# Kernel optimization log

Measured on AMD Instinct MI355X. Metric: run time of the kernel, lower is better.

Reference implementation:

```python
import jax, jax.numpy as jnp
import numpy as np

NUM_CAPS = 16; PLANES = 16; CAPS_SIZE = 16; NUM_CLASSES = 10
MAT = 4; ITERS = 3; FINAL_LAMBDA = 1e-2; EPS = 1e-8; BN_EPS = 1e-5
LN_2PI = float(np.log(2.0 * np.pi))


def _conv(x, w, pad):
    return jax.lax.conv_general_dilated(x, w, (1, 1), ((pad, pad), (pad, pad)),
                                        dimension_numbers=('NCHW', 'OIHW', 'NCHW'))


def _bn(x, g, b, m, v):
    # inference-mode BatchNorm2d
    scale = g / jnp.sqrt(v + BN_EPS)
    return (x - m[None, :, None, None]) * scale[None, :, None, None] + b[None, :, None, None]


def _unfold(x, k, stride, pad):
    # torch F.unfold ordering: [b, c, k*k, l]
    b, c, h, w = x.shape
    xp = jnp.pad(x, ((0, 0), (0, 0), (pad, pad), (pad, pad)))
    oh = (h + 2 * pad - k) // stride + 1
    ow = (w + 2 * pad - k) // stride + 1
    cols = jnp.stack([xp[:, :, i:i + stride * (oh - 1) + 1:stride, j:j + stride * (ow - 1) + 1:stride]
                      for i in range(k) for j in range(k)], axis=2)  # [b,c,kk,oh,ow]
    return cols.reshape(b, c, k * k, oh * ow), oh, ow


def em_routing(a, pose, W, beta_u, beta_a, k, stride, pad, A, B, P):
    mat = int(P ** 0.5); b = a.shape[0]; kk = k * k
    pc, oh, ow = _unfold(pose, k, stride, pad)          # [b, A*P, kk, l]
    l = oh * ow
    pc = pc.reshape(b, A, P, kk, l)
    pc = jnp.transpose(pc, (0, 4, 3, 1, 2)).reshape(b, l, kk * A, mat, mat)
    # votes: [b, l, kkA, B, P]
    v = jnp.einsum('blkih,kohj->blkoij', pc, W).reshape(b, l, kk * A, B, P)
    ac, _, _ = _unfold(a, k, stride, pad)               # [b, A, kk, l]
    a_in = jnp.transpose(ac.reshape(b, A, kk, l), (0, 3, 2, 1)).reshape(b, l, kk * A, 1)
    bu = beta_u.reshape(1, 1, 1, B, 1)
    ba = beta_a.reshape(1, 1, 1, B)
    r = jnp.full((b, l, kk * A, B), 1.0 / B, dtype=a.dtype)
    for it in range(ITERS):
        lam = FINAL_LAMBDA * (1.0 - 0.95 ** (it + 1))
        # ---- M step ----
        rw = r * a_in
        rw = rw / (jnp.sum(rw, axis=3, keepdims=True) + EPS)
        r_sum = jnp.sum(rw, axis=2, keepdims=True)            # [b,l,1,B]
        coeff = (rw / (r_sum + EPS))[..., None]
        mu = jnp.sum(coeff * v, axis=2, keepdims=True)        # [b,l,1,B,P]
        sig = jnp.sum(coeff * (v - mu) ** 2, axis=2, keepdims=True) + EPS
        cost = (bu + 0.5 * jnp.log(sig)) * r_sum[..., None]
        a_out = jax.nn.sigmoid(lam * (ba - jnp.sum(cost, axis=4)))  # [b,l,1,B]
        # ---- E step ----
        if it < ITERS - 1:
            ln_p = -0.5 * (v - mu) ** 2 / sig - 0.5 * jnp.log(sig) - 0.5 * LN_2PI
            r = jax.nn.softmax(jnp.sum(ln_p, axis=4) + jnp.log(a_out), axis=3)
    a_map = jnp.transpose(a_out.reshape(b, oh, ow, B), (0, 3, 1, 2))
    pose_map = jnp.transpose(mu.reshape(b, oh, ow, B * P), (0, 3, 1, 2))
    return a_map, pose_map


def setup_inputs() -> dict:
    key = jax.random.key(0)
    ks = jax.random.split(key, 24)
    Bt = 32; C_in = NUM_CAPS * PLANES  # 256
    d = {}
    d['x'] = jax.random.normal(ks[0], (Bt, C_in, 8, 8), jnp.float32)
    d['conv_a_w'] = jax.random.normal(ks[1], (NUM_CAPS, C_in, 3, 3), jnp.float32) * 0.03
    d['conv_pose_w'] = jax.random.normal(ks[2], (NUM_CAPS * CAPS_SIZE, C_in, 3, 3), jnp.float32) * 0.03

    def bn_params(k1, k2, c):
        return (jnp.ones((c,), jnp.float32), jnp.zeros((c,), jnp.float32),
                jax.random.normal(k1, (c,), jnp.float32) * 0.1,
                1.0 + 0.1 * jax.random.uniform(k2, (c,), jnp.float32))
    d['bn_a_g'], d['bn_a_b'], d['bn_a_m'], d['bn_a_v'] = bn_params(ks[3], ks[4], NUM_CAPS)
    d['bn_pose_g'], d['bn_pose_b'], d['bn_pose_m'], d['bn_pose_v'] = bn_params(ks[5], ks[6], NUM_CAPS * CAPS_SIZE)
    kkA = 9 * NUM_CAPS
    d['em0_W'] = jax.random.uniform(ks[7], (kkA, NUM_CAPS, MAT, MAT), jnp.float32, -0.5, 0.5)
    d['em0_bu'] = jax.random.normal(ks[8], (NUM_CAPS,), jnp.float32) * 0.01
    d['em0_ba'] = jax.random.normal(ks[9], (NUM_CAPS,), jnp.float32) * 0.01
    d['bn0_g'], d['bn0_b'], d['bn0_m'], d['bn0_v'] = bn_params(ks[10], ks[11], NUM_CAPS * CAPS_SIZE)
    d['em1_W'] = jax.random.uniform(ks[12], (kkA, NUM_CAPS, MAT, MAT), jnp.float32, -0.5, 0.5)
    d['em1_bu'] = jax.random.normal(ks[13], (NUM_CAPS,), jnp.float32) * 0.01
    d['em1_ba'] = jax.random.normal(ks[14], (NUM_CAPS,), jnp.float32) * 0.01
    d['bn1_g'], d['bn1_b'], d['bn1_m'], d['bn1_v'] = bn_params(ks[15], ks[16], NUM_CAPS * CAPS_SIZE)
    d['fc_W'] = jax.random.uniform(ks[17], (16 * NUM_CAPS, NUM_CLASSES, MAT, MAT), jnp.float32, -0.5, 0.5)
    d['fc_bu'] = jax.random.normal(ks[18], (NUM_CLASSES,), jnp.float32) * 0.01
    d['fc_ba'] = jax.random.normal(ks[19], (NUM_CLASSES,), jnp.float32) * 0.01
    return d


def reference(x, conv_a_w, conv_pose_w, bn_a_g, bn_a_b, bn_a_m, bn_a_v,
              bn_pose_g, bn_pose_b, bn_pose_m, bn_pose_v,
              em0_W, em0_bu, em0_ba, bn0_g, bn0_b, bn0_m, bn0_v,
              em1_W, em1_bu, em1_ba, bn1_g, bn1_b, bn1_m, bn1_v,
              fc_W, fc_bu, fc_ba):
    a = jax.nn.sigmoid(_bn(_conv(x, conv_a_w, 1), bn_a_g, bn_a_b, bn_a_m, bn_a_v))
    pose = _bn(_conv(x, conv_pose_w, 1), bn_pose_g, bn_pose_b, bn_pose_m, bn_pose_v)
    a, pose = em_routing(a, pose, em0_W, em0_bu, em0_ba, 3, 1, 1, NUM_CAPS, NUM_CAPS, CAPS_SIZE)
    pose = _bn(pose, bn0_g, bn0_b, bn0_m, bn0_v)
    a, pose = em_routing(a, pose, em1_W, em1_bu, em1_ba, 3, 1, 1, NUM_CAPS, NUM_CAPS, CAPS_SIZE)
    pose = _bn(pose, bn1_g, bn1_b, bn1_m, bn1_v)
    a, _ = em_routing(a, pose, fc_W, fc_bu, fc_ba, 4, 1, 0, NUM_CAPS, NUM_CLASSES, CAPS_SIZE)
    return jnp.mean(a, axis=(2, 3))  # [B, num_classes]
```

## Files before the change

kernel.cpp:

```cpp
#include <hip/hip_runtime.h>

#define EPSV 1e-8f
#define BN_EPS 1e-5f
#define LN_2PI 1.8378770664093453f

typedef float v2f __attribute__((ext_vector_type(2)));
__device__ __forceinline__ v2f splat2(float x) { v2f r; r.x = x; r.y = x; return r; }

__device__ __forceinline__ float sigmoidf_(float x) { return 1.0f / (1.0f + expf(-x)); }

template<int C>
__device__ __forceinline__ float dppx(float x) {
    int i = __builtin_amdgcn_mov_dpp(__builtin_bit_cast(int, x), C, 0xF, 0xF, true);
    return __builtin_bit_cast(float, i);
}


template<int NACC>
__device__ __forceinline__ void conv3_body(
    const float* __restrict__ x, const float* __restrict__ w,
    const float* __restrict__ g, const float* __restrict__ b_,
    const float* __restrict__ m, const float* __restrict__ v,
    float* __restrict__ out, int OC, int icChunk,
    int bidx, int ocg, int icq, float* xs, int t)
{
    const int pix = t & 63, py = pix >> 3, px = pix & 7;
    const int ocb_u = __builtin_amdgcn_readfirstlane(t >> 6);
    const int ic0 = icq * icChunk;
    const int OCB = 4 * NACC;

    const int cells = icChunk * 120;
    for (int idx = t; idx < cells; idx += 256) {
        int icl = idx / 120;
        int c = idx - icl * 120;
        int iy = c / 12, ix = c - iy * 12;
        float val = 0.f;
        if (iy >= 1 && iy <= 8 && ix >= 1 && ix <= 8)
            val = x[(bidx * 256 + ic0 + icl) * 64 + (iy - 1) * 8 + (ix - 1)];
        xs[idx] = val;
    }
    __syncthreads();

    const int oc_base = ocg * OCB + ocb_u;
    const float* wb = w + ((size_t)(oc_base * 256 + ic0)) * 9;

    float acc[NACC];
    #pragma unroll
    for (int q = 0; q < NACC; ++q) acc[q] = 0.f;

    for (int icl = 0; icl < icChunk; ++icl) {
        const float* xr = &xs[icl * 120 + py * 12 + px];
        const float* wr = &wb[icl * 9];
        #pragma unroll
        for (int ky = 0; ky < 3; ++ky)
            #pragma unroll
            for (int kx = 0; kx < 3; ++kx) {
                float xv = xr[ky * 12 + kx];
                #pragma unroll
                for (int q = 0; q < NACC; ++q)
                    acc[q] = fmaf(wr[q * 9216 + ky * 3 + kx], xv, acc[q]);
            }
    }
    __syncthreads();
    #pragma unroll
    for (int q = 0; q < NACC; ++q) {
        int oc = oc_base + 4 * q;
        float sc = g[oc] * rsqrtf(v[oc] + BN_EPS);
        float add = acc[q] * sc;
        if (icq == 0) add += b_[oc] - m[oc] * sc;
        xs[pix * (OCB + 1) + ocb_u + 4 * q] = add;
    }
    __syncthreads();
    const int per = (64 * OCB) / 256;
    #pragma unroll
    for (int e = 0; e < per; ++e) {
        int idx = t * per + e;
        int pp = idx / OCB, ocl = idx - pp * OCB;
        atomicAdd(&out[(bidx * 64 + pp) * OC + ocg * OCB + ocl], xs[pp * (OCB + 1) + ocl]);
    }
}

__global__ __launch_bounds__(256, 4) void k_conv_fused(
    const float* __restrict__ x,
    const float* __restrict__ wa, const float* __restrict__ ga, const float* __restrict__ bba,
    const float* __restrict__ ma, const float* __restrict__ va, float* __restrict__ outa,
    const float* __restrict__ wp, const float* __restrict__ gp, const float* __restrict__ bbp,
    const float* __restrict__ mp, const float* __restrict__ vp, float* __restrict__ outp)
{
    __shared__ float xs[32 * 120];
    const int t = threadIdx.x;
    const int bid = blockIdx.x;
    if (bid < 256) {
        int bidx = bid >> 3, icq = bid & 7;
        conv3_body<4>(x, wa, ga, bba, ma, va, outa, 16, 32, bidx, 0, icq, xs, t);
    } else {
        int r = bid - 256;
        int bidx = r >> 6, rem = r & 63;
        int ocg = rem >> 3, icq = rem & 7;
        conv3_body<8>(x, wp, gp, bbp, mp, vp, outp, 256, 32, bidx, ocg, icq, xs, t);
    }
}

__global__ __launch_bounds__(768) void k_em_conv(
    const float* __restrict__ a_in, const float* __restrict__ pose_in,
    const float* __restrict__ W, const float* __restrict__ bu, const float* __restrict__ ba,
    const float* __restrict__ bng, const float* __restrict__ bnb,
    const float* __restrict__ bnm, const float* __restrict__ bnv,
    float* __restrict__ a_out_g, float* __restrict__ pose_out, int sig_flag)
{
    __shared__ float4 red4[192 * 9] __attribute__((aligned(16)));
    __shared__ float prsum[192];
    __shared__ float a_s[160];
    __shared__ float mu_s[16 * 18], is_s[16 * 18];
    __shared__ float cst0_s[16], aout_s[16], laout_s[16];

    const int t = threadIdx.x;
    const int bidx = blockIdx.x >> 6;
    const int l = blockIdx.x & 63;
    const int y = l >> 3, xo = l & 7;
    const int kgl = t & 3;
    const int o = (t >> 2) & 15;
    const int w_id = t >> 6;
    const int kg = w_id * 4 + kgl;

    float* pc_s = reinterpret_cast<float*>(red4);

    for (int idx = t; idx < 2304; idx += 768) {
        int kk = idx >> 8, c = idx & 255;
        int k = idx >> 4, p = idx & 15;
        int iy = y + kk / 3 - 1, ix = xo + (kk % 3) - 1;
        float val = 0.f;
        if (iy >= 0 && iy < 8 && ix >= 0 && ix < 8)
            val = pose_in[((bidx * 64 + iy * 8 + ix) << 8) + c];
        pc_s[k * 20 + p] = val;
    }
    if (t < 144) {
        int kk = t >> 4;
        int iy = y + kk / 3 - 1, ix = xo + (kk % 3) - 1;
        float raw = (iy >= 0 && iy < 8 && ix >= 0 && ix < 8)
                    ? a_in[((bidx * 64 + iy * 8 + ix) << 4) + (t & 15)] : 0.f;
        a_s[t] = sig_flag ? sigmoidf_(raw) : raw;
    }
    __syncthreads();

    v2f v2[3][8];
    const float4* W4 = reinterpret_cast<const float4*>(W);
    #pragma unroll
    for (int s = 0; s < 3; ++s) {
        int k = kg + 48 * s;
        float pcl[16];
        #pragma unroll
        for (int c = 0; c < 4; ++c) {
            float4 p4 = *reinterpret_cast<const float4*>(&pc_s[k * 20 + c * 4]);
            pcl[c * 4 + 0] = p4.x; pcl[c * 4 + 1] = p4.y; pcl[c * 4 + 2] = p4.z; pcl[c * 4 + 3] = p4.w;
        }
        #pragma unroll
        for (int j = 0; j < 8; ++j) v2[s][j] = splat2(0.f);
        #pragma unroll
        for (int h = 0; h < 4; ++h) {
            float4 wr = W4[(k * 16 + o) * 4 + h];
            v2f wa; wa.x = wr.x; wa.y = wr.y;
            v2f wb; wb.x = wr.z; wb.y = wr.w;
            #pragma unroll
            for (int i = 0; i < 4; ++i) {
                v2f a2 = splat2(pcl[i * 4 + h]);
                v2[s][i * 2]     += a2 * wa;
                v2[s][i * 2 + 1] += a2 * wb;
            }
        }
    }
    float afac[3];
    #pragma unroll
    for (int s = 0; s < 3; ++s) { float av = a_s[kg + 48 * s]; afac[s] = av / (av + EPSV); }
    __syncthreads();

    float lg[3] = {0.f, 0.f, 0.f};
    for (int it = 0; it < 3; ++it) {
        float lam = (it == 0) ? 5.0e-4f : ((it == 1) ? 9.75e-4f : 1.42625e-3f);
        float rw[3];
        if (it == 0) {
            #pragma unroll
            for (int s = 0; s < 3; ++s) rw[s] = 0.0625f * afac[s];
        } else {
            #pragma unroll
            for (int s = 0; s < 3; ++s) {
                float mx = lg[s];
                #pragma unroll
                for (int mk = 4; mk <= 32; mk <<= 1) mx = fmaxf(mx, __shfl_xor(mx, mk, 64));
                float e = expf(lg[s] - mx);
                float den = e;
                #pragma unroll
                for (int mk = 4; mk <= 32; mk <<= 1) den += __shfl_xor(den, mk, 64);
                rw[s] = (e / den) * afac[s];
            }
        }
        float prw = rw[0] + rw[1] + rw[2];
        prw += dppx<0xB1>(prw); prw += dppx<0x4E>(prw);
        if (kgl == 0) prsum[w_id * 16 + o] = prw;
        const int row4 = (w_id * 16 + o) * 9;
        const v2f r0 = splat2(rw[0]), r1 = splat2(rw[1]), r2 = splat2(rw[2]);
        #pragma unroll
        for (int j = 0; j < 8; ++j) {
            v2f a0 = v2[0][j], a1 = v2[1][j], a2 = v2[2][j];
            v2f pm = r0 * a0 + r1 * a1 + r2 * a2;
            v2f pq = r0 * (a0 * a0) + r1 * (a1 * a1) + r2 * (a2 * a2);
            float pmx = pm.x, pmy = pm.y, pqx = pq.x, pqy = pq.y;
            pmx += dppx<0xB1>(pmx); pmx += dppx<0x4E>(pmx);
            pmy += dppx<0xB1>(pmy); pmy += dppx<0x4E>(pmy);
            pqx += dppx<0xB1>(pqx); pqx += dppx<0x4E>(pqx);
            pqy += dppx<0xB1>(pqy); pqy += dppx<0x4E>(pqy);
            if (kgl == 0) red4[row4 + j] = make_float4(pmx, pmy, pqx, pqy);
        }
        __syncthreads();
        if (t < 256) {
            int oo = t >> 4, p = t & 15;
            int jj = p >> 1, sel = p & 1;
            const float* rf = reinterpret_cast<const float*>(red4);
            float spm = 0.f, spq = 0.f, srs = 0.f;
            #pragma unroll
            for (int u = 0; u < 12; ++u) {
                int base = ((u * 16 + oo) * 9 + jj) * 4;
                spm += rf[base + sel];
                spq += rf[base + 2 + sel];
                srs += prsum[u * 16 + oo];
            }
            float invr = 1.f / (srs + EPSV);
            float mu = spm * invr;
            float beta = srs * invr;
            float sig = fmaf(-(2.f - beta) * mu, mu, spq * invr) + EPSV;
            float ls = logf(sig);
            mu_s[oo * 18 + p] = mu;
            is_s[oo * 18 + p] = 1.f / sig;
            float sumls = ls;
            #pragma unroll
            for (int mk = 1; mk <= 8; mk <<= 1) sumls += __shfl_xor(sumls, mk, 64);
            if (p == 0) {
                float cost = srs * fmaf(0.5f, sumls, 16.f * bu[oo]);
                float ao = sigmoidf_(lam * (ba[oo] - cost));
                aout_s[oo] = ao; laout_s[oo] = logf(ao);
                cst0_s[oo] = fmaf(-0.5f, sumls, -8.f * LN_2PI);
            }
        }
        __syncthreads();
        if (it < 2) {
            const v2f* mu2 = reinterpret_cast<const v2f*>(&mu_s[o * 18]);
            const v2f* is2 = reinterpret_cast<const v2f*>(&is_s[o * 18]);
            v2f s0 = splat2(0.f), s1 = splat2(0.f), s2 = splat2(0.f);
            #pragma unroll
            for (int j = 0; j < 8; ++j) {
                v2f m2 = mu2[j], iv = is2[j];
                v2f d0 = v2[0][j] - m2; s0 += (d0 * d0) * iv;
                v2f d1 = v2[1][j] - m2; s1 += (d1 * d1) * iv;
                v2f d2 = v2[2][j] - m2; s2 += (d2 * d2) * iv;
            }
            float cb = cst0_s[o] + laout_s[o];
            lg[0] = fmaf(-0.5f, s0.x + s0.y, cb);
            lg[1] = fmaf(-0.5f, s1.x + s1.y, cb);
            lg[2] = fmaf(-0.5f, s2.x + s2.y, cb);
        }
    }
    if (t < 256) {
        float sc = bng[t] * rsqrtf(bnv[t] + BN_EPS);
        float mu = mu_s[(t >> 4) * 18 + (t & 15)];
        pose_out[((bidx * 64 + l) << 8) + t] = (mu - bnm[t]) * sc + bnb[t];
    }
    if (t < 16) a_out_g[((bidx * 64 + l) << 4) + t] = aout_s[t];
}

__global__ __launch_bounds__(640) void k_em_fc(
    const float* __restrict__ a_in, const float* __restrict__ pose_in,
    const float* __restrict__ W, const float* __restrict__ bu, const float* __restrict__ ba,
    float* __restrict__ out)
{
    __shared__ float pcs[5120];
    __shared__ float rws[2816];
    __shared__ float ain_s[256];
    __shared__ float mu_s[10 * 18], is_s[10 * 18];

    const int t = threadIdx.x;
    const int bidx = blockIdx.x / 25;
    const int l = blockIdx.x % 25;
    const int y = l / 5, xo = l % 5;
    const int o = t >> 6;
    const int g = t & 63;

    for (int idx = t; idx < 4096; idx += 640) {
        int kk = idx >> 8, c = idx & 255;
        int k = idx >> 4, p = idx & 15;
        int iy = y + (kk >> 2), ix = xo + (kk & 3);
        pcs[k * 20 + p] = pose_in[((bidx * 64 + iy * 8 + ix) << 8) + c];
    }
    if (t < 256) {
        int kk = t >> 4;
        int iy = y + (kk >> 2), ix = xo + (kk & 3);
        ain_s[t] = a_in[((bidx * 64 + iy * 8 + ix) << 4) + (t & 15)];
    }
    __syncthreads();

    v2f v2[4][8];
    const float4* W4 = reinterpret_cast<const float4*>(W);
    #pragma unroll
    for (int s = 0; s < 4; ++s) {
        int k = g + 64 * s;
        float pcl[16];
        #pragma unroll
        for (int c = 0; c < 4; ++c) {
            float4 p4 = *reinterpret_cast<const float4*>(&pcs[k * 20 + c * 4]);
            pcl[c * 4 + 0] = p4.x; pcl[c * 4 + 1] = p4.y; pcl[c * 4 + 2] = p4.z; pcl[c * 4 + 3] = p4.w;
        }
        #pragma unroll
        for (int j = 0; j < 8; ++j) v2[s][j] = splat2(0.f);
        #pragma unroll
        for (int h = 0; h < 4; ++h) {
            float4 wr = W4[(k * 10 + o) * 4 + h];
            v2f wa; wa.x = wr.x; wa.y = wr.y;
            v2f wb; wb.x = wr.z; wb.y = wr.w;
            #pragma unroll
            for (int i = 0; i < 4; ++i) {
                v2f a2 = splat2(pcl[i * 4 + h]);
                v2[s][i * 2]     += a2 * wa;
                v2[s][i * 2 + 1] += a2 * wb;
            }
        }
    }

    const float bu_o = bu[o], ba_o = ba[o];
    const int myp = (g >> 2) & 15;
    float aout_f = 0.f;

    for (int it = 0; it < 3; ++it) {
        float lam = (it == 0) ? 5.0e-4f : ((it == 1) ? 9.75e-4f : 1.42625e-3f);
        if (t < 256) {
            float av = ain_s[t];
            if (it == 0) {
                float val = 0.1f * av / (av + EPSV);
                #pragma unroll
                for (int oo = 0; oo < 10; ++oo) rws[t * 11 + oo] = val;
            } else {
                float mx = -1e30f;
                #pragma unroll
                for (int oo = 0; oo < 10; ++oo) mx = fmaxf(mx, rws[t * 11 + oo]);
                float den = 0.f;
                #pragma unroll
                for (int oo = 0; oo < 10; ++oo) den += expf(rws[t * 11 + oo] - mx);
                float sc = av / (den * (av + EPSV));
                #pragma unroll
                for (int oo = 0; oo < 10; ++oo) rws[t * 11 + oo] = expf(rws[t * 11 + oo] - mx) * sc;
            }
        }
        __syncthreads();
        float rwl[4]; float rs = 0.f;
        #pragma unroll
        for (int s = 0; s < 4; ++s) { rwl[s] = rws[(g + 64 * s) * 11 + o]; rs += rwl[s]; }
        #pragma unroll
        for (int mk = 1; mk <= 32; mk <<= 1) rs += __shfl_xor(rs, mk, 64);
        const float invr = 1.f / (rs + EPSV);
        const float beta = rs * invr;
        const v2f q0 = splat2(rwl[0]), q1 = splat2(rwl[1]), q2 = splat2(rwl[2]), q3 = splat2(rwl[3]);
        float mu_p;
        {
            float cur[16];
            #pragma unroll
            for (int j = 0; j < 8; ++j) {
                v2f pm = q0 * v2[0][j] + q1 * v2[1][j] + q2 * v2[2][j] + q3 * v2[3][j];
                cur[2 * j] = pm.x; cur[2 * j + 1] = pm.y;
            }
            { const bool hi = (g & 32) != 0;
              #pragma unroll
              for (int i = 0; i < 8; ++i) {
                  float send = hi ? cur[i] : cur[i + 8];
                  float keep = hi ? cur[i + 8] : cur[i];
                  cur[i] = keep + __shfl_xor(send, 32, 64);
              } }
            { const bool hi = (g & 16) != 0;
              #pragma unroll
              for (int i = 0; i < 4; ++i) {
                  float send = hi ? cur[i] : cur[i + 4];
                  float keep = hi ? cur[i + 4] : cur[i];
                  cur[i] = keep + __shfl_xor(send, 16, 64);
              } }
            { const bool hi = (g & 8) != 0;
              #pragma unroll
              for (int i = 0; i < 2; ++i) {
                  float send = hi ? cur[i] : cur[i + 2];
                  float keep = hi ? cur[i + 2] : cur[i];
                  cur[i] = keep + __shfl_xor(send, 8, 64);
              } }
            { const bool hi = (g & 4) != 0;
              float send = hi ? cur[0] : cur[1];
              float keep = hi ? cur[1] : cur[0];
              cur[0] = keep + __shfl_xor(send, 4, 64); }
            float r = cur[0];
            r += __shfl_xor(r, 1, 64);
            r += __shfl_xor(r, 2, 64);
            mu_p = r * invr;
        }
        if ((g & 3) == 0) mu_s[o * 18 + myp] = mu_p;
        float ls;
        {
            float cur[16];
            #pragma unroll
            for (int j = 0; j < 8; ++j) {
                v2f a0 = v2[0][j], a1 = v2[1][j], a2 = v2[2][j], a3 = v2[3][j];
                v2f pq = q0 * (a0 * a0) + q1 * (a1 * a1) + q2 * (a2 * a2) + q3 * (a3 * a3);
                cur[2 * j] = pq.x; cur[2 * j + 1] = pq.y;
            }
            { const bool hi = (g & 32) != 0;
              #pragma unroll
              for (int i = 0; i < 8; ++i) {
                  float send = hi ? cur[i] : cur[i + 8];
                  float keep = hi ? cur[i + 8] : cur[i];
                  cur[i] = keep + __shfl_xor(send, 32, 64);
              } }
            { const bool hi = (g & 16) != 0;
              #pragma unroll
              for (int i = 0; i < 4; ++i) {
                  float send = hi ? cur[i] : cur[i + 4];
                  float keep = hi ? cur[i + 4] : cur[i];
                  cur[i] = keep + __shfl_xor(send, 16, 64);
              } }
            { const bool hi = (g & 8) != 0;
              #pragma unroll
              for (int i = 0; i < 2; ++i) {
                  float send = hi ? cur[i] : cur[i + 2];
                  float keep = hi ? cur[i + 2] : cur[i];
                  cur[i] = keep + __shfl_xor(send, 8, 64);
              } }
            { const bool hi = (g & 4) != 0;
              float send = hi ? cur[0] : cur[1];
              float keep = hi ? cur[1] : cur[0];
              cur[0] = keep + __shfl_xor(send, 4, 64); }
            float r = cur[0];
            r += __shfl_xor(r, 1, 64);
            r += __shfl_xor(r, 2, 64);
            float E2 = r * invr;
            float sig = fmaf(-(2.f - beta) * mu_p, mu_p, E2) + EPSV;
            ls = logf(sig);
            if ((g & 3) == 0) is_s[o * 18 + myp] = 1.f / sig;
        }
        float sumls = ls;
        #pragma unroll
        for (int mk = 4; mk <= 32; mk <<= 1) sumls += __shfl_xor(sumls, mk, 64);
        float cost = rs * fmaf(0.5f, sumls, 16.f * bu_o);
        float ao = sigmoidf_(lam * (ba_o - cost));
        if (it == 2) aout_f = ao;
        if (it < 2) {
            float cst = fmaf(-0.5f, sumls, -8.f * LN_2PI) + logf(ao);
            const v2f* mu2 = reinterpret_cast<const v2f*>(&mu_s[o * 18]);
            const v2f* is2 = reinterpret_cast<const v2f*>(&is_s[o * 18]);
            v2f s0 = splat2(0.f), s1 = splat2(0.f), s2 = splat2(0.f), s3 = splat2(0.f);
            #pragma unroll
            for (int j = 0; j < 8; ++j) {
                v2f m2 = mu2[j], iv = is2[j];
                v2f d0 = v2[0][j] - m2; s0 += (d0 * d0) * iv;
                v2f d1 = v2[1][j] - m2; s1 += (d1 * d1) * iv;
                v2f d2 = v2[2][j] - m2; s2 += (d2 * d2) * iv;
                v2f d3 = v2[3][j] - m2; s3 += (d3 * d3) * iv;
            }
            rws[(g      ) * 11 + o] = fmaf(-0.5f, s0.x + s0.y, cst);
            rws[(g +  64) * 11 + o] = fmaf(-0.5f, s1.x + s1.y, cst);
            rws[(g + 128) * 11 + o] = fmaf(-0.5f, s2.x + s2.y, cst);
            rws[(g + 192) * 11 + o] = fmaf(-0.5f, s3.x + s3.y, cst);
            __syncthreads();
        }
    }
    if (g == 0) atomicAdd(&out[bidx * 10 + o], aout_f * 0.04f);
}

extern "C" void kernel_launch(void* const* d_in, const int* in_sizes, int n_in,
                              void* d_out, int out_size, void* d_ws, size_t ws_size,
                              hipStream_t stream)
{
    const float* x           = (const float*)d_in[0];
    const float* conv_a_w    = (const float*)d_in[1];
    const float* conv_pose_w = (const float*)d_in[2];
    const float* bn_a_g = (const float*)d_in[3];
    const float* bn_a_b = (const float*)d_in[4];
    const float* bn_a_m = (const float*)d_in[5];
    const float* bn_a_v = (const float*)d_in[6];
    const float* bn_p_g = (const float*)d_in[7];
    const float* bn_p_b = (const float*)d_in[8];
    const float* bn_p_m = (const float*)d_in[9];
    const float* bn_p_v = (const float*)d_in[10];
    const float* em0_W  = (const float*)d_in[11];
    const float* em0_bu = (const float*)d_in[12];
    const float* em0_ba = (const float*)d_in[13];
    const float* bn0_g  = (const float*)d_in[14];
    const float* bn0_b  = (const float*)d_in[15];
    const float* bn0_m  = (const float*)d_in[16];
    const float* bn0_v  = (const float*)d_in[17];
    const float* em1_W  = (const float*)d_in[18];
    const float* em1_bu = (const float*)d_in[19];
    const float* em1_ba = (const float*)d_in[20];
    const float* bn1_g  = (const float*)d_in[21];
    const float* bn1_b  = (const float*)d_in[22];
    const float* bn1_m  = (const float*)d_in[23];
    const float* bn1_v  = (const float*)d_in[24];
    const float* fc_W   = (const float*)d_in[25];
    const float* fc_bu  = (const float*)d_in[26];
    const float* fc_ba  = (const float*)d_in[27];

    float* ws    = (float*)d_ws;
    float* a0    = ws;
    float* pose0 = a0 + 32768;
    float* a1    = pose0 + 524288;
    float* pose1 = a1 + 32768;
    float* a2    = pose1 + 524288;
    float* pose2 = a2 + 32768;
    float* out   = (float*)d_out;

    hipMemsetAsync(d_out, 0, (size_t)out_size * sizeof(float), stream);
    hipMemsetAsync(a0, 0, (size_t)(32768 + 524288) * sizeof(float), stream);
    k_conv_fused<<<2304, 256, 0, stream>>>(x,
        conv_a_w, bn_a_g, bn_a_b, bn_a_m, bn_a_v, a0,
        conv_pose_w, bn_p_g, bn_p_b, bn_p_m, bn_p_v, pose0);
    k_em_conv<<<2048, 768, 0, stream>>>(a0, pose0, em0_W, em0_bu, em0_ba,
                                        bn0_g, bn0_b, bn0_m, bn0_v, a1, pose1, 1);
    k_em_conv<<<2048, 768, 0, stream>>>(a1, pose1, em1_W, em1_bu, em1_ba,
                                        bn1_g, bn1_b, bn1_m, bn1_v, a2, pose2, 0);
    k_em_fc<<<800, 640, 0, stream>>>(a2, pose2, fc_W, fc_bu, fc_ba, out);
}
```

Baseline: 537.1 us.

## Drop split-K in fused conv, use full-channel blocks with direct stores

The fused conv kernel no longer splits the 256 input channels across 8 blocks. Each block now loops over the channels in two staged chunks of 128 and writes its BN-scaled result with plain stores instead of atomicAdd, which also makes the workspace memset unnecessary. This is meant to remove atomic traffic and the extra memset launch. In exchange the grid shrinks from 2304 to 288 blocks, each with 8x more serial work and a much larger shared-memory footprint, which cuts parallelism and occupancy.

```diff
diff --git a/kernel.cpp b/kernel.cpp
--- a/kernel.cpp
+++ b/kernel.cpp
@@ -21,62 +21,60 @@
     const float* __restrict__ x, const float* __restrict__ w,
     const float* __restrict__ g, const float* __restrict__ b_,
     const float* __restrict__ m, const float* __restrict__ v,
-    float* __restrict__ out, int OC, int icChunk,
-    int bidx, int ocg, int icq, float* xs, int t)
+    float* __restrict__ out, int OC,
+    int bidx, int ocg, float* xs, int t)
 {
     const int pix = t & 63, py = pix >> 3, px = pix & 7;
     const int ocb_u = __builtin_amdgcn_readfirstlane(t >> 6);
-    const int ic0 = icq * icChunk;
     const int OCB = 4 * NACC;
-
-    const int cells = icChunk * 120;
-    for (int idx = t; idx < cells; idx += 256) {
-        int icl = idx / 120;
-        int c = idx - icl * 120;
-        int iy = c / 12, ix = c - iy * 12;
-        float val = 0.f;
-        if (iy >= 1 && iy <= 8 && ix >= 1 && ix <= 8)
-            val = x[(bidx * 256 + ic0 + icl) * 64 + (iy - 1) * 8 + (ix - 1)];
-        xs[idx] = val;
-    }
-    __syncthreads();
-
-    const int oc_base = ocg * OCB + ocb_u;
-    const float* wb = w + ((size_t)(oc_base * 256 + ic0)) * 9;
 
     float acc[NACC];
     #pragma unroll
     for (int q = 0; q < NACC; ++q) acc[q] = 0.f;
 
-    for (int icl = 0; icl < icChunk; ++icl) {
-        const float* xr = &xs[icl * 120 + py * 12 + px];
-        const float* wr = &wb[icl * 9];
-        #pragma unroll
-        for (int ky = 0; ky < 3; ++ky)
-            #pragma unroll
-            for (int kx = 0; kx < 3; ++kx) {
-                float xv = xr[ky * 12 + kx];
-                #pragma unroll
-                for (int q = 0; q < NACC; ++q)
-                    acc[q] = fmaf(wr[q * 9216 + ky * 3 + kx], xv, acc[q]);
-            }
+    for (int ch = 0; ch < 2; ++ch) {
+        const int ic0 = ch * 128;
+        if (ch) __syncthreads();
+        for (int idx = t; idx < 128 * 120; idx += 256) {
+            int icl = idx / 120;
+            int c = idx - icl * 120;
+            int iy = c / 12, ix = c - iy * 12;
+            float val = 0.f;
+            if (iy >= 1 && iy <= 8 && ix >= 1 && ix <= 8)
+                val = x[(bidx * 256 + ic0 + icl) * 64 + (iy - 1) * 8 + (ix - 1)];
+            xs[idx] = val;
+        }
+        __syncthreads();
+
+        const float* wb = w + ((size_t)(ocg * OCB + ocb_u) * 256 + ic0) * 9;
+        for (int icl = 0; icl < 128; ++icl) {
+            const float* xr = &xs[icl * 120 + py * 12 + px];
+            const float* wr = &wb[icl * 9];
+            #pragma unroll
+            for (int ky = 0; ky < 3; ++ky)
+                #pragma unroll
+                for (int kx = 0; kx < 3; ++kx) {
+                    float xv = xr[ky * 12 + kx];
+                    #pragma unroll
+                    for (int q = 0; q < NACC; ++q)
+                        acc[q] = fmaf(wr[q * 9216 + ky * 3 + kx], xv, acc[q]);
+                }
+        }
     }
     __syncthreads();
     #pragma unroll
     for (int q = 0; q < NACC; ++q) {
-        int oc = oc_base + 4 * q;
+        int oc = ocg * OCB + ocb_u + 4 * q;
         float sc = g[oc] * rsqrtf(v[oc] + BN_EPS);
-        float add = acc[q] * sc;
-        if (icq == 0) add += b_[oc] - m[oc] * sc;
-        xs[pix * (OCB + 1) + ocb_u + 4 * q] = add;
+        xs[pix * (OCB + 1) + ocb_u + 4 * q] = fmaf(acc[q], sc, b_[oc] - m[oc] * sc);
     }
     __syncthreads();
     const int per = (64 * OCB) / 256;
     #pragma unroll
     for (int e = 0; e < per; ++e) {
-        int idx = t * per + e;
+        int idx = e * 256 + t;
         int pp = idx / OCB, ocl = idx - pp * OCB;
-        atomicAdd(&out[(bidx * 64 + pp) * OC + ocg * OCB + ocl], xs[pp * (OCB + 1) + ocl]);
+        out[(bidx * 64 + pp) * OC + ocg * OCB + ocl] = xs[pp * (OCB + 1) + ocl];
     }
 }
 
@@ -87,17 +85,15 @@
     const float* __restrict__ wp, const float* __restrict__ gp, const float* __restrict__ bbp,
     const float* __restrict__ mp, const float* __restrict__ vp, float* __restrict__ outp)
 {
-    __shared__ float xs[32 * 120];
+    __shared__ float xs[128 * 120];
     const int t = threadIdx.x;
     const int bid = blockIdx.x;
     if (bid < 256) {
-        int bidx = bid >> 3, icq = bid & 7;
-        conv3_body<4>(x, wa, ga, bba, ma, va, outa, 16, 32, bidx, 0, icq, xs, t);
+        int bidx = bid >> 3, ocg = bid & 7;
+        conv3_body<8>(x, wp, gp, bbp, mp, vp, outp, 256, bidx, ocg, xs, t);
     } else {
-        int r = bid - 256;
-        int bidx = r >> 6, rem = r & 63;
-        int ocg = rem >> 3, icq = rem & 7;
-        conv3_body<8>(x, wp, gp, bbp, mp, vp, outp, 256, 32, bidx, ocg, icq, xs, t);
+        int bidx = bid - 256;
+        conv3_body<4>(x, wa, ga, bba, ma, va, outa, 16, bidx, 0, xs, t);
     }
 }
 
@@ -510,8 +506,7 @@
     float* out   = (float*)d_out;
 
     hipMemsetAsync(d_out, 0, (size_t)out_size * sizeof(float), stream);
-    hipMemsetAsync(a0, 0, (size_t)(32768 + 524288) * sizeof(float), stream);
-    k_conv_fused<<<2304, 256, 0, stream>>>(x,
+    k_conv_fused<<<288, 256, 0, stream>>>(x,
         conv_a_w, bn_a_g, bn_a_b, bn_a_m, bn_a_v, a0,
         conv_pose_w, bn_p_g, bn_p_b, bn_p_m, bn_p_v, pose0);
     k_em_conv<<<2048, 768, 0, stream>>>(a0, pose0, em0_W, em0_bu, em0_ba,
```

After: 540.7 us. Within noise of the previous version (+0.7%).
